# Optimization experiments

Hardware: AMD Instinct MI355X
Metric: run time of the kernel (lower is better)

Reference implementation:

```python
import jax, jax.numpy as jnp
import numpy as np

B, N, C = 8, 1374, 768
H = 12
HD = C // H  # 64
HIDDEN = int(C * 4.0)  # 3072
EPS = 1e-5


def setup_inputs() -> dict:
    key = jax.random.key(0)
    ks = jax.random.split(key, 12)
    s = 0.02
    return {
        "x": jax.random.normal(ks[0], (B, N, C), jnp.float32),
        "rope_freqs": jax.random.normal(ks[1], (1, N, 1, HD), jnp.float32),
        "ln1_g": jnp.ones((C,), jnp.float32),
        "ln1_b": jnp.zeros((C,), jnp.float32),
        "qkv_w": jax.random.normal(ks[2], (3 * C, C), jnp.float32) * s,
        "qkv_b": jnp.zeros((3 * C,), jnp.float32),
        "proj_w": jax.random.normal(ks[3], (C, C), jnp.float32) * s,
        "proj_b": jnp.zeros((C,), jnp.float32),
        "ln2_g": jnp.ones((C,), jnp.float32),
        "ln2_b": jnp.zeros((C,), jnp.float32),
        "w1": jax.random.normal(ks[4], (HIDDEN, C), jnp.float32) * s,
        "b1": jnp.zeros((HIDDEN,), jnp.float32),
        "w2": jax.random.normal(ks[5], (HIDDEN, C), jnp.float32) * s,
        "b2": jnp.zeros((HIDDEN,), jnp.float32),
        "w3": jax.random.normal(ks[6], (C, HIDDEN), jnp.float32) * s,
        "b3": jnp.zeros((C,), jnp.float32),
    }


def _layernorm(x, g, b):
    mu = jnp.mean(x, axis=-1, keepdims=True)
    var = jnp.mean(jnp.square(x - mu), axis=-1, keepdims=True)
    return (x - mu) * jax.lax.rsqrt(var + EPS) * g + b


def _rotate_half(x):
    x1, x2 = jnp.split(x, 2, axis=-1)
    return jnp.concatenate([-x2, x1], axis=-1)


def _apply_rope(q, k, freqs):
    # freqs: [1, N, 1, HD] -> [1, 1, N, HD] (matches torch permute(0,2,1,3))
    f = jnp.transpose(freqs, (0, 2, 1, 3))
    cos, sin = jnp.cos(f), jnp.sin(f)
    q_rot = q * cos + _rotate_half(q) * sin
    k_rot = k * cos + _rotate_half(k) * sin
    return q_rot, k_rot


def reference(x, rope_freqs, ln1_g, ln1_b, qkv_w, qkv_b, proj_w, proj_b,
              ln2_g, ln2_b, w1, b1, w2, b2, w3, b3):
    scale = HD ** -0.5
    # --- Attention branch ---
    h = _layernorm(x, ln1_g, ln1_b)
    qkv = jnp.einsum('bnc,dc->bnd', h, qkv_w) + qkv_b          # [B,N,3C]
    qkv = qkv.reshape(B, N, 3, H, HD).transpose(2, 0, 3, 1, 4)  # [3,B,H,N,HD]
    q, k, v = qkv[0], qkv[1], qkv[2]
    # rope_freqs covers all N tokens -> n_special = 0 path
    q, k = _apply_rope(q, k, rope_freqs)
    attn = jnp.einsum('bhnd,bhmd->bhnm', q, k) * scale          # [B,H,N,N]
    attn = jax.nn.softmax(attn, axis=-1)
    o = jnp.einsum('bhnm,bhmd->bhnd', attn, v)                  # [B,H,N,HD]
    o = o.transpose(0, 2, 1, 3).reshape(B, N, C)
    o = jnp.einsum('bnc,dc->bnd', o, proj_w) + proj_b
    x = x + o
    # --- SwiGLU MLP branch ---
    h2 = _layernorm(x, ln2_g, ln2_b)
    x1 = jnp.einsum('bnc,hc->bnh', h2, w1) + b1
    x2 = jnp.einsum('bnc,hc->bnh', h2, w2) + b2
    hid = jax.nn.silu(x1) * x2
    mlp_out = jnp.einsum('bnh,ch->bnc', hid, w3) + b3
    return x + mlp_out
```

## Files before the change

kernel.cpp:

```cpp
#include <hip/hip_runtime.h>
#include <stdint.h>

#define B_ 8
#define N_ 1374
#define C_ 768
#define H_ 12
#define HD_ 64
#define HID_ 3072
#define M_ (B_*N_)
#define MPAD_ 11008
#define QT_ 22
#define QT2_ 11

#define QSC_ 0.18033688011112042f

typedef __attribute__((ext_vector_type(8))) short short8;
typedef __attribute__((ext_vector_type(4))) float f32x4;
typedef __attribute__((ext_vector_type(16))) float f32x16;
typedef __attribute__((ext_vector_type(4))) _Float16 half4;
typedef __attribute__((ext_vector_type(2))) _Float16 half2v;

__device__ __forceinline__ unsigned short f2bf(float f) {
  unsigned u = __float_as_uint(f);
  u += 0x7FFF + ((u >> 16) & 1);
  return (unsigned short)(u >> 16);
}
__device__ __forceinline__ float bf2f(unsigned short h) {
  return __uint_as_float(((unsigned)h) << 16);
}
__device__ __forceinline__ unsigned short f2h(float f) {
  return __builtin_bit_cast(unsigned short, (_Float16)f);
}

__device__ __forceinline__ half2v pkrtz(float a, float b) {
  return __builtin_bit_cast(half2v, __builtin_amdgcn_cvt_pkrtz(a, b));
}

#if __has_builtin(__builtin_amdgcn_global_load_lds)
#define HAVE_GLL 1
#endif

__device__ __forceinline__ void gld16(const unsigned short* g, unsigned short* l) {
#ifdef HAVE_GLL
  __builtin_amdgcn_global_load_lds((const __attribute__((address_space(1))) void*)g,
                                   (__attribute__((address_space(3))) void*)l, 16, 0, 0);
#else
  *(short8*)l = *(const short8*)g;
#endif
}

__global__ __launch_bounds__(256) void cvt5_kernel(
    const float* __restrict__ s0, const float* __restrict__ s1,
    const float* __restrict__ s2, const float* __restrict__ s3,
    const float* __restrict__ s4, unsigned short* __restrict__ out) {
  int id = blockIdx.x * 256 + threadIdx.x;
  const float* src; int off;
  if (id < 442368)        { src = s0; off = id; }
  else if (id < 589824)   { src = s1; off = id - 442368; }
  else if (id < 1179648)  { src = s2; off = id - 589824; }
  else if (id < 1769472)  { src = s3; off = id - 1179648; }
  else                    { src = s4; off = id - 1769472; }
  float4 v = ((const float4*)src)[off];
  ushort4 o;
  o.x = f2bf(v.x); o.y = f2bf(v.y); o.z = f2bf(v.z); o.w = f2bf(v.w);
  ((ushort4*)out)[id] = o;
}

__global__ __launch_bounds__(256) void ln_kernel(const float* __restrict__ in,
    const float* __restrict__ g, const float* __restrict__ bta,
    unsigned short* __restrict__ out) {
  int row = blockIdx.x;
  int t = threadIdx.x;
  const float* xr = in + (size_t)row * C_;
  float v0 = xr[t], v1 = xr[t + 256], v2 = xr[t + 512];
  float s1 = v0 + v1 + v2;
  float s2 = v0*v0 + v1*v1 + v2*v2;
  for (int off = 1; off < 64; off <<= 1) {
    s1 += __shfl_xor(s1, off, 64);
    s2 += __shfl_xor(s2, off, 64);
  }
  __shared__ float r1[4], r2[4];
  int wave = t >> 6, lane = t & 63;
  if (lane == 0) { r1[wave] = s1; r2[wave] = s2; }
  __syncthreads();
  float tot1 = r1[0] + r1[1] + r1[2] + r1[3];
  float tot2 = r2[0] + r2[1] + r2[2] + r2[3];
  float mu = tot1 * (1.0f / C_);
  float var = tot2 * (1.0f / C_) - mu * mu;
  float rs = rsqrtf(var + 1e-5f);
  size_t ob = (size_t)row * C_;
  out[ob + t]       = f2bf((v0 - mu) * rs * g[t]       + bta[t]);
  out[ob + t + 256] = f2bf((v1 - mu) * rs * g[t + 256] + bta[t + 256]);
  out[ob + t + 512] = f2bf((v2 - mu) * rs * g[t + 512] + bta[t + 512]);
}

template<int EPI, int ROPE, int TM, int SWZ>
__global__ __launch_bounds__(256, (TM == 64) ? 4 : 2) void gemm_bt(
    const unsigned short* __restrict__ A,
    const unsigned short* __restrict__ W,
    void* __restrict__ outp,
    const float* __restrict__ bias0,
    const float* __restrict__ resid,
    const float* __restrict__ freqs,
    int K, int ldo, int Mvalid, int X)
{
  constexpr int MI = TM / 32;
  __shared__ __align__(16) unsigned short As[2][TM * 32];
  __shared__ __align__(16) unsigned short Bs[2][4096];
  const int t = threadIdx.x;
  const int lane = t & 63;
  const int wave = t >> 6;
  const int wm = (wave >> 1) * (TM / 2);
  const int wn = (wave & 1) * 64;
  const int lr = lane & 15;
  const int lg = lane >> 4;
  const int lk = lg * 8;
  int bx, by;
  if (SWZ) {
    int Y = gridDim.x / X;
    int lin = blockIdx.x;
    int sgsz = X * 8;
    int sg = lin / sgsz;
    int base_y = sg * 8;
    int rows = Y - base_y; if (rows > 8) rows = 8;
    int within = lin - sg * sgsz;
    by = base_y + within % rows;
    bx = within / rows;
  } else {
    bx = blockIdx.x % X;
    by = blockIdx.x / X;
  }
  const int tm0 = by * TM;
  const int tn0 = bx * 128;
  const int r0 = t >> 2;
  const int c0 = (t & 3) * 8;
  const unsigned short* ga0 = A + (size_t)(tm0 + r0) * K + c0;
  const unsigned short* ga1 = A + (size_t)(tm0 + 64 + r0) * K + c0;
  const unsigned short* gb0 = W + (size_t)(tn0 + r0) * K + c0;
  const unsigned short* gb1 = W + (size_t)(tn0 + 64 + r0) * K + c0;
  f32x4 zero = {0.f, 0.f, 0.f, 0.f};
  f32x4 acc[MI][4];
#pragma unroll
  for (int mi = 0; mi < MI; ++mi)
#pragma unroll
    for (int ni = 0; ni < 4; ++ni) acc[mi][ni] = zero;

  for (int kt = 0; kt < K; kt += 64) {
    __syncthreads();
    gld16(ga0 + kt,      &As[0][t * 8]);
    gld16(ga0 + kt + 32, &As[1][t * 8]);
    if (TM == 128) {
      gld16(ga1 + kt,      &As[0][2048 + t * 8]);
      gld16(ga1 + kt + 32, &As[1][2048 + t * 8]);
    }
    gld16(gb0 + kt,      &Bs[0][t * 8]);
    gld16(gb1 + kt,      &Bs[0][2048 + t * 8]);
    gld16(gb0 + kt + 32, &Bs[1][t * 8]);
    gld16(gb1 + kt + 32, &Bs[1][2048 + t * 8]);
    __syncthreads();
#pragma unroll
    for (int u = 0; u < 2; ++u) {
      short8 af[MI], bfr[4];
#pragma unroll
      for (int mi = 0; mi < MI; ++mi) af[mi] = *(const short8*)&As[u][(wm + mi * 16 + lr) * 32 + lk];
#pragma unroll
      for (int ni = 0; ni < 4; ++ni) bfr[ni] = *(const short8*)&Bs[u][(wn + ni * 16 + lr) * 32 + lk];
#pragma unroll
      for (int mi = 0; mi < MI; ++mi)
#pragma unroll
        for (int ni = 0; ni < 4; ++ni)
          acc[mi][ni] = __builtin_amdgcn_mfma_f32_16x16x32_bf16(af[mi], bfr[ni], acc[mi][ni], 0, 0, 0);
    }
  }

  if (EPI == 0) {
    bool dorope = ROPE && ((tn0 + wn) < 1536);
    bool isq    = ROPE && ((tn0 + wn) < 768);
    bool isv    = ROPE && ((tn0 + wn) >= 1536);
#pragma unroll
    for (int mi = 0; mi < MI; ++mi) {
#pragma unroll
      for (int p = 0; p < 2; ++p) {
        int col1 = tn0 + wn + p * 16 + lr;
        int col2 = col1 + 32;
        float bv1 = bias0[col1], bv2 = bias0[col2];
        int e = p * 16 + lr;
#pragma unroll
        for (int r = 0; r < 4; ++r) {
          int row = tm0 + wm + mi * 16 + lg * 4 + r;
          float v1 = acc[mi][p][r] + bv1;
          float v2 = acc[mi][p + 2][r] + bv2;
          float o1 = v1, o2 = v2;
          if (dorope) {
            int n = row % N_;
            float f1 = freqs[n * HD_ + e];
            float f2 = freqs[n * HD_ + e + 32];
            float c1, s1, c2, s2;
            __sincosf(f1, &s1, &c1);
            __sincosf(f2, &s2, &c2);
            o1 = v1 * c1 - v2 * s1;
            o2 = v2 * c2 + v1 * s2;
          }
          if (isq) { o1 *= QSC_; o2 *= QSC_; }
          size_t base = (size_t)row * ldo;
          if (isv) {
            ((unsigned short*)outp)[base + col1] = f2h(o1);
            ((unsigned short*)outp)[base + col2] = f2h(o2);
          } else {
            ((unsigned short*)outp)[base + col1] = f2bf(o1);
            ((unsigned short*)outp)[base + col2] = f2bf(o2);
          }
        }
      }
    }
  } else {
#pragma unroll
    for (int mi = 0; mi < MI; ++mi) {
#pragma unroll
      for (int ni = 0; ni < 4; ++ni) {
        int col = tn0 + wn + ni * 16 + lr;
        float bval = bias0[col];
#pragma unroll
        for (int r = 0; r < 4; ++r) {
          int row = tm0 + wm + mi * 16 + lg * 4 + r;
          float v = acc[mi][ni][r] + bval;
          size_t idx = (size_t)row * ldo + col;
          if (EPI == 1) {
            if (row < Mvalid) ((float*)outp)[idx] = resid[idx] + v;
          } else {
            if (row < Mvalid) ((float*)outp)[idx] = ((float*)outp)[idx] + v;
          }
        }
      }
    }
  }
}

__global__ __launch_bounds__(256, 2) void gemm_w12_swiglu(
    const unsigned short* __restrict__ A,
    const unsigned short* __restrict__ W1,
    const unsigned short* __restrict__ W2,
    unsigned short* __restrict__ hid,
    const float* __restrict__ b1,
    const float* __restrict__ b2)
{
  __shared__ __align__(16) unsigned short As[2][4096];
  __shared__ __align__(16) unsigned short B1s[2][2048];
  __shared__ __align__(16) unsigned short B2s[2][2048];
  const int t = threadIdx.x;
  const int lane = t & 63;
  const int wave = t >> 6;
  const int wm = (wave >> 1) * 64;
  const int wn = (wave & 1) * 32;
  const int lr = lane & 15;
  const int lg = lane >> 4;
  const int lk = lg * 8;
  const int tm0 = blockIdx.y * 128;
  const int tn0 = blockIdx.x * 64;
  const int r0 = t >> 2;
  const int c0 = (t & 3) * 8;
  const unsigned short* ga0 = A + (size_t)(tm0 + r0) * 768 + c0;
  const unsigned short* ga1 = A + (size_t)(tm0 + 64 + r0) * 768 + c0;
  const unsigned short* g1 = W1 + (size_t)(tn0 + r0) * 768 + c0;
  const unsigned short* g2 = W2 + (size_t)(tn0 + r0) * 768 + c0;
  f32x4 zero = {0.f, 0.f, 0.f, 0.f};
  f32x4 acc1[4][2], acc2[4][2];
#pragma unroll
  for (int mi = 0; mi < 4; ++mi)
#pragma unroll
    for (int ni = 0; ni < 2; ++ni) { acc1[mi][ni] = zero; acc2[mi][ni] = zero; }

  for (int kt = 0; kt < 768; kt += 64) {
    __syncthreads();
    gld16(ga0 + kt,      &As[0][t * 8]);
    gld16(ga1 + kt,      &As[0][2048 + t * 8]);
    gld16(ga0 + kt + 32, &As[1][t * 8]);
    gld16(ga1 + kt + 32, &As[1][2048 + t * 8]);
    gld16(g1 + kt,       &B1s[0][t * 8]);
    gld16(g1 + kt + 32,  &B1s[1][t * 8]);
    gld16(g2 + kt,       &B2s[0][t * 8]);
    gld16(g2 + kt + 32,  &B2s[1][t * 8]);
    __syncthreads();
#pragma unroll
    for (int u = 0; u < 2; ++u) {
      short8 af[4], b1f[2], b2f[2];
#pragma unroll
      for (int mi = 0; mi < 4; ++mi) af[mi] = *(const short8*)&As[u][(wm + mi * 16 + lr) * 32 + lk];
#pragma unroll
      for (int ni = 0; ni < 2; ++ni) {
        b1f[ni] = *(const short8*)&B1s[u][(wn + ni * 16 + lr) * 32 + lk];
        b2f[ni] = *(const short8*)&B2s[u][(wn + ni * 16 + lr) * 32 + lk];
      }
#pragma unroll
      for (int mi = 0; mi < 4; ++mi)
#pragma unroll
        for (int ni = 0; ni < 2; ++ni) {
          acc1[mi][ni] = __builtin_amdgcn_mfma_f32_16x16x32_bf16(af[mi], b1f[ni], acc1[mi][ni], 0, 0, 0);
          acc2[mi][ni] = __builtin_amdgcn_mfma_f32_16x16x32_bf16(af[mi], b2f[ni], acc2[mi][ni], 0, 0, 0);
        }
    }
  }
#pragma unroll
  for (int mi = 0; mi < 4; ++mi) {
#pragma unroll
    for (int ni = 0; ni < 2; ++ni) {
      int col = tn0 + wn + ni * 16 + lr;
      float bv1 = b1[col], bv2 = b2[col];
#pragma unroll
      for (int r = 0; r < 4; ++r) {
        int row = tm0 + wm + mi * 16 + lg * 4 + r;
        float a1 = acc1[mi][ni][r] + bv1;
        float a2 = acc2[mi][ni][r] + bv2;
        float h = a1 / (1.f + __expf(-a1)) * a2;
        hid[(size_t)row * HID_ + col] = f2bf(h);
      }
    }
  }
}

struct FalseT { static constexpr bool value = false; };
struct TrueT  { static constexpr bool value = true;  };

__global__ __launch_bounds__(256, 3) void attn_kernel(
    const unsigned short* __restrict__ qkv,
    unsigned short* __restrict__ o2)
{
  __shared__ __align__(16) unsigned short Ks[2][64 * 88];
  __shared__ __align__(16) _Float16 Vt[2][64 * 72];
  int bidx = blockIdx.x;
  int qt = bidx % QT2_;
  int bh = bidx / QT2_;
  int head = bh % H_;
  int b = bh / H_;
  int t = threadIdx.x, lane = t & 63, wave = t >> 6;
  int lq = lane & 31, lg2 = lane >> 5;

  short8 bq[4];
  {
    int m = qt * 128 + wave * 32 + lq;
    int mc = (m < N_) ? m : (N_ - 1);
    const unsigned short* qrow = qkv + (size_t)(b * N_ + mc) * 2304 + head * HD_;
#pragma unroll
    for (int c = 0; c < 4; ++c)
      bq[c] = *(const short8*)(qrow + c * 16 + lg2 * 8);
  }

  f32x16 acc[2];
  f32x16 dacc;
  acc[0] = {}; acc[1] = {}; dacc = {};

  const int kr0 = t >> 3;
  const int kc  = (t & 7) * 8;
  const int vp  = t & 31;
  const int vc  = t >> 5;
  const unsigned short* kbase = qkv + (size_t)(b * N_) * 2304 + 768  + head * HD_ + kc;
  const unsigned short* vbase = qkv + (size_t)(b * N_) * 2304 + 1536 + head * HD_ + vc * 8;

  short8 krg[2], vrg[2];
  auto issue = [&](int jt) {
    int j0 = jt * 64 + kr0;        if (j0 >= N_) j0 = N_ - 1;
    int j1 = jt * 64 + kr0 + 32;   if (j1 >= N_) j1 = N_ - 1;
    int vj0 = jt * 64 + 2 * vp;    if (vj0 >= N_) vj0 = N_ - 1;
    int vj1 = jt * 64 + 2 * vp + 1; if (vj1 >= N_) vj1 = N_ - 1;
    krg[0] = *(const short8*)(kbase + (size_t)j0 * 2304);
    krg[1] = *(const short8*)(kbase + (size_t)j1 * 2304);
    vrg[0] = *(const short8*)(vbase + (size_t)vj0 * 2304);
    vrg[1] = *(const short8*)(vbase + (size_t)vj1 * 2304);
  };

  const half4 vones = {(_Float16)1.f, (_Float16)1.f, (_Float16)1.f, (_Float16)1.f};

  auto compute = [&](int jt, const unsigned short* ksb, const _Float16* vtb, auto tailc) {
    constexpr bool TAIL = decltype(tailc)::value;
#pragma unroll
    for (int st2 = 0; st2 < 2; ++st2) {
      f32x16 sc = {};
      {
        const unsigned short* krow = &ksb[(st2 * 32 + lq) * 88 + lg2 * 8];
        short8 ak0 = *(const short8*)(krow);
        short8 ak1 = *(const short8*)(krow + 16);
        short8 ak2 = *(const short8*)(krow + 32);
        short8 ak3 = *(const short8*)(krow + 48);
        sc = __builtin_amdgcn_mfma_f32_32x32x16_bf16(ak0, bq[0], sc, 0, 0, 0);
        sc = __builtin_amdgcn_mfma_f32_32x32x16_bf16(ak1, bq[1], sc, 0, 0, 0);
        sc = __builtin_amdgcn_mfma_f32_32x32x16_bf16(ak2, bq[2], sc, 0, 0, 0);
        sc = __builtin_amdgcn_mfma_f32_32x32x16_bf16(ak3, bq[3], sc, 0, 0, 0);
      }
#pragma unroll
      for (int r = 0; r < 16; ++r) {
        float pv = exp2f(sc[r]);
        if (TAIL) {
          int jw = (r & 3) + 8 * (r >> 2) + 4 * lg2;
          int j = jt * 64 + st2 * 32 + jw;
          pv = (j < N_) ? pv : 0.f;
        }
        sc[r] = pv;
      }
      half4 pf[4];
#pragma unroll
      for (int ks = 0; ks < 4; ++ks) {
        union { half4 v; half2v h[2]; } pu;
        pu.h[0] = pkrtz(sc[ks * 4 + 0], sc[ks * 4 + 1]);
        pu.h[1] = pkrtz(sc[ks * 4 + 2], sc[ks * 4 + 3]);
        pf[ks] = pu.v;
      }
#pragma unroll
      for (int ks = 0; ks < 4; ++ks)
        dacc = __builtin_amdgcn_mfma_f32_32x32x8f16(pf[ks], vones, dacc, 0, 0, 0);
#pragma unroll
      for (int dt = 0; dt < 2; ++dt) {
#pragma unroll
        for (int ks = 0; ks < 4; ++ks) {
          half4 bv = *(const half4*)&vtb[(dt * 32 + lq) * 72 + st2 * 32 + ks * 8 + lg2 * 4];
          acc[dt] = __builtin_amdgcn_mfma_f32_32x32x8f16(pf[ks], bv, acc[dt], 0, 0, 0);
        }
      }
    }
  };

  issue(0);
  int cur = 0;
  for (int jt = 0; jt < QT_; ++jt) {
    unsigned short* ksb = &Ks[cur][0];
    _Float16* vtb = &Vt[cur][0];
    *(short8*)&ksb[kr0 * 88 + kc] = krg[0];
    *(short8*)&ksb[(kr0 + 32) * 88 + kc] = krg[1];
#pragma unroll
    for (int i = 0; i < 8; ++i) {
      unsigned lo = (unsigned short)vrg[0][i];
      unsigned hi = (unsigned short)vrg[1][i];
      *(unsigned*)&Vt[cur][(vc * 8 + i) * 72 + 2 * vp] = lo | (hi << 16);
    }
    __syncthreads();
    issue(jt + 1);
    if (jt == QT_ - 1) compute(jt, ksb, vtb, TrueT{});
    else               compute(jt, ksb, vtb, FalseT{});
    cur ^= 1;
  }

#pragma unroll
  for (int r = 0; r < 16; ++r) {
    int qw = (r & 3) + 8 * (r >> 2) + 4 * lg2;
    int m = qt * 128 + wave * 32 + qw;
    if (m < N_) {
      float invd = 1.f / dacc[r];
      unsigned short* orow = o2 + (size_t)(b * N_ + m) * C_ + head * HD_ + lq;
      orow[0]  = f2bf(acc[0][r] * invd);
      orow[32] = f2bf(acc[1][r] * invd);
    }
  }
}

extern "C" void kernel_launch(void* const* d_in, const int* in_sizes, int n_in,
                              void* d_out, int out_size, void* d_ws, size_t ws_size,
                              hipStream_t stream) {
  const float* x      = (const float*)d_in[0];
  const float* freqs  = (const float*)d_in[1];
  const float* ln1_g  = (const float*)d_in[2];
  const float* ln1_b  = (const float*)d_in[3];
  const float* qkv_w  = (const float*)d_in[4];
  const float* qkv_b  = (const float*)d_in[5];
  const float* proj_w = (const float*)d_in[6];
  const float* proj_b = (const float*)d_in[7];
  const float* ln2_g  = (const float*)d_in[8];
  const float* ln2_b  = (const float*)d_in[9];
  const float* w1     = (const float*)d_in[10];
  const float* b1     = (const float*)d_in[11];
  const float* w2     = (const float*)d_in[12];
  const float* b2     = (const float*)d_in[13];
  const float* w3     = (const float*)d_in[14];
  const float* b3     = (const float*)d_in[15];
  float* out = (float*)d_out;
  char* ws = (char*)d_ws;

  unsigned short* hB     = (unsigned short*)(ws + 0);
  unsigned short* wqkvB  = (unsigned short*)(ws + 16908288);
  unsigned short* wprojB = (unsigned short*)(ws + 20447232);
  unsigned short* w12B   = (unsigned short*)(ws + 21626880);
  unsigned short* w3B    = (unsigned short*)(ws + 31064064);
  unsigned short* qkvB   = (unsigned short*)(ws + 35782656);
  unsigned short* o2B    = (unsigned short*)(ws + 86507520);
  unsigned short* hidB   = qkvB;

  cvt5_kernel<<<9216, 256, 0, stream>>>(qkv_w, proj_w, w1, w2, w3, wqkvB);

  ln_kernel<<<M_, 256, 0, stream>>>(x, ln1_g, ln1_b, hB);
  gemm_bt<0, 1, 128, 1><<<18 * 86, 256, 0, stream>>>(hB, wqkvB, qkvB, qkv_b, nullptr, freqs, 768, 2304, M_, 18);
  attn_kernel<<<B_ * H_ * QT2_, 256, 0, stream>>>(qkvB, o2B);
  gemm_bt<1, 0, 64, 1><<<6 * 172, 256, 0, stream>>>(o2B, wprojB, out, proj_b, x, nullptr, 768, 768, M_, 6);

  ln_kernel<<<M_, 256, 0, stream>>>(out, ln2_g, ln2_b, hB);
  gemm_w12_swiglu<<<dim3(48, 86), 256, 0, stream>>>(hB, w12B, w12B + 3072 * 768, hidB, b1, b2);
  gemm_bt<3, 0, 128, 1><<<6 * 86, 256, 0, stream>>>(hidB, w3B, out, b3, nullptr, nullptr, 3072, 768, M_, 6);
}
```

Baseline: 534.5 us.

## Double-buffer LDS tiles in GEMM kernels to overlap global loads with MFMA

Both the generic GEMM and the fused W1/W2 SwiGLU GEMM now keep two LDS stages. The next K-tile is issued into the alternate buffer while MFMAs run on the current one, which also drops one barrier per iteration. The goal is to hide global-to-LDS load latency behind compute. The cost is double the LDS footprint per block, so the TM=64 launch bound drops from 4 to 3 blocks per CU, which can reduce occupancy.

```diff
diff --git a/kernel.cpp b/kernel.cpp
--- a/kernel.cpp
+++ b/kernel.cpp
@@ -95,7 +95,7 @@
 }
 
 template<int EPI, int ROPE, int TM, int SWZ>
-__global__ __launch_bounds__(256, (TM == 64) ? 4 : 2) void gemm_bt(
+__global__ __launch_bounds__(256, (TM == 64) ? 3 : 2) void gemm_bt(
     const unsigned short* __restrict__ A,
     const unsigned short* __restrict__ W,
     void* __restrict__ outp,
@@ -105,8 +105,8 @@
     int K, int ldo, int Mvalid, int X)
 {
   constexpr int MI = TM / 32;
-  __shared__ __align__(16) unsigned short As[2][TM * 32];
-  __shared__ __align__(16) unsigned short Bs[2][4096];
+  __shared__ __align__(16) unsigned short As[2][2][TM * 32];
+  __shared__ __align__(16) unsigned short Bs[2][2][4096];
   const int t = threadIdx.x;
   const int lane = t & 63;
   const int wave = t >> 6;
@@ -138,6 +138,20 @@
   const unsigned short* ga1 = A + (size_t)(tm0 + 64 + r0) * K + c0;
   const unsigned short* gb0 = W + (size_t)(tn0 + r0) * K + c0;
   const unsigned short* gb1 = W + (size_t)(tn0 + 64 + r0) * K + c0;
+
+  auto stage = [&](int buf, int kt) {
+    gld16(ga0 + kt,      &As[buf][0][t * 8]);
+    gld16(ga0 + kt + 32, &As[buf][1][t * 8]);
+    if (TM == 128) {
+      gld16(ga1 + kt,      &As[buf][0][2048 + t * 8]);
+      gld16(ga1 + kt + 32, &As[buf][1][2048 + t * 8]);
+    }
+    gld16(gb0 + kt,      &Bs[buf][0][t * 8]);
+    gld16(gb1 + kt,      &Bs[buf][0][2048 + t * 8]);
+    gld16(gb0 + kt + 32, &Bs[buf][1][t * 8]);
+    gld16(gb1 + kt + 32, &Bs[buf][1][2048 + t * 8]);
+  };
+
   f32x4 zero = {0.f, 0.f, 0.f, 0.f};
   f32x4 acc[MI][4];
 #pragma unroll
@@ -145,32 +159,25 @@
 #pragma unroll
     for (int ni = 0; ni < 4; ++ni) acc[mi][ni] = zero;
 
+  stage(0, 0);
+  int cur = 0;
   for (int kt = 0; kt < K; kt += 64) {
     __syncthreads();
-    gld16(ga0 + kt,      &As[0][t * 8]);
-    gld16(ga0 + kt + 32, &As[1][t * 8]);
-    if (TM == 128) {
-      gld16(ga1 + kt,      &As[0][2048 + t * 8]);
-      gld16(ga1 + kt + 32, &As[1][2048 + t * 8]);
-    }
-    gld16(gb0 + kt,      &Bs[0][t * 8]);
-    gld16(gb1 + kt,      &Bs[0][2048 + t * 8]);
-    gld16(gb0 + kt + 32, &Bs[1][t * 8]);
-    gld16(gb1 + kt + 32, &Bs[1][2048 + t * 8]);
-    __syncthreads();
+    if (kt + 64 < K) stage(cur ^ 1, kt + 64);
 #pragma unroll
     for (int u = 0; u < 2; ++u) {
       short8 af[MI], bfr[4];
 #pragma unroll
-      for (int mi = 0; mi < MI; ++mi) af[mi] = *(const short8*)&As[u][(wm + mi * 16 + lr) * 32 + lk];
-#pragma unroll
-      for (int ni = 0; ni < 4; ++ni) bfr[ni] = *(const short8*)&Bs[u][(wn + ni * 16 + lr) * 32 + lk];
+      for (int mi = 0; mi < MI; ++mi) af[mi] = *(const short8*)&As[cur][u][(wm + mi * 16 + lr) * 32 + lk];
+#pragma unroll
+      for (int ni = 0; ni < 4; ++ni) bfr[ni] = *(const short8*)&Bs[cur][u][(wn + ni * 16 + lr) * 32 + lk];
 #pragma unroll
       for (int mi = 0; mi < MI; ++mi)
 #pragma unroll
         for (int ni = 0; ni < 4; ++ni)
           acc[mi][ni] = __builtin_amdgcn_mfma_f32_16x16x32_bf16(af[mi], bfr[ni], acc[mi][ni], 0, 0, 0);
     }
+    cur ^= 1;
   }
 
   if (EPI == 0) {
@@ -244,9 +251,9 @@
     const float* __restrict__ b1,
     const float* __restrict__ b2)
 {
-  __shared__ __align__(16) unsigned short As[2][4096];
-  __shared__ __align__(16) unsigned short B1s[2][2048];
-  __shared__ __align__(16) unsigned short B2s[2][2048];
+  __shared__ __align__(16) unsigned short As[2][2][4096];
+  __shared__ __align__(16) unsigned short B1s[2][2][2048];
+  __shared__ __align__(16) unsigned short B2s[2][2][2048];
   const int t = threadIdx.x;
   const int lane = t & 63;
   const int wave = t >> 6;
@@ -263,6 +270,18 @@
   const unsigned short* ga1 = A + (size_t)(tm0 + 64 + r0) * 768 + c0;
   const unsigned short* g1 = W1 + (size_t)(tn0 + r0) * 768 + c0;
   const unsigned short* g2 = W2 + (size_t)(tn0 + r0) * 768 + c0;
+
+  auto stage = [&](int buf, int kt) {
+    gld16(ga0 + kt,      &As[buf][0][t * 8]);
+    gld16(ga1 + kt,      &As[buf][0][2048 + t * 8]);
+    gld16(ga0 + kt + 32, &As[buf][1][t * 8]);
+    gld16(ga1 + kt + 32, &As[buf][1][2048 + t * 8]);
+    gld16(g1 + kt,       &B1s[buf][0][t * 8]);
+    gld16(g1 + kt + 32,  &B1s[buf][1][t * 8]);
+    gld16(g2 + kt,       &B2s[buf][0][t * 8]);
+    gld16(g2 + kt + 32,  &B2s[buf][1][t * 8]);
+  };
+
   f32x4 zero = {0.f, 0.f, 0.f, 0.f};
   f32x4 acc1[4][2], acc2[4][2];
 #pragma unroll
@@ -270,26 +289,20 @@
 #pragma unroll
     for (int ni = 0; ni < 2; ++ni) { acc1[mi][ni] = zero; acc2[mi][ni] = zero; }
 
+  stage(0, 0);
+  int cur = 0;
   for (int kt = 0; kt < 768; kt += 64) {
     __syncthreads();
-    gld16(ga0 + kt,      &As[0][t * 8]);
-    gld16(ga1 + kt,      &As[0][2048 + t * 8]);
-    gld16(ga0 + kt + 32, &As[1][t * 8]);
-    gld16(ga1 + kt + 32, &As[1][2048 + t * 8]);
-    gld16(g1 + kt,       &B1s[0][t * 8]);
-    gld16(g1 + kt + 32,  &B1s[1][t * 8]);
-    gld16(g2 + kt,       &B2s[0][t * 8]);
-    gld16(g2 + kt + 32,  &B2s[1][t * 8]);
-    __syncthreads();
+    if (kt + 64 < 768) stage(cur ^ 1, kt + 64);
 #pragma unroll
     for (int u = 0; u < 2; ++u) {
       short8 af[4], b1f[2], b2f[2];
 #pragma unroll
-      for (int mi = 0; mi < 4; ++mi) af[mi] = *(const short8*)&As[u][(wm + mi * 16 + lr) * 32 + lk];
+      for (int mi = 0; mi < 4; ++mi) af[mi] = *(const short8*)&As[cur][u][(wm + mi * 16 + lr) * 32 + lk];
 #pragma unroll
       for (int ni = 0; ni < 2; ++ni) {
-        b1f[ni] = *(const short8*)&B1s[u][(wn + ni * 16 + lr) * 32 + lk];
-        b2f[ni] = *(const short8*)&B2s[u][(wn + ni * 16 + lr) * 32 + lk];
+        b1f[ni] = *(const short8*)&B1s[cur][u][(wn + ni * 16 + lr) * 32 + lk];
+        b2f[ni] = *(const short8*)&B2s[cur][u][(wn + ni * 16 + lr) * 32 + lk];
       }
 #pragma unroll
       for (int mi = 0; mi < 4; ++mi)
@@ -299,6 +312,7 @@
           acc2[mi][ni] = __builtin_amdgcn_mfma_f32_16x16x32_bf16(af[mi], b2f[ni], acc2[mi][ni], 0, 0, 0);
         }
     }
+    cur ^= 1;
   }
 #pragma unroll
   for (int mi = 0; mi < 4; ++mi) {
```

Result: slower. 643.1 us (+20.3%).

## Double-buffer LDS tiles in the GEMM and SwiGLU kernels to overlap loads with MFMA

Applied to the files above, without the earlier changes.

The main GEMM and the fused SwiGLU up-projection kernel now use a software-pipelined K loop. The two LDS buffers hold consecutive 32-wide K slices instead of two halves of one 64-wide slice. Each iteration issues the global-to-LDS loads for the next slice and then runs MFMAs on the current one, with a single barrier per step. The goal is to hide global load latency behind matrix math. The cost is twice as many loop iterations and barriers, and each step has less MFMA work to cover the load latency.

```diff
diff --git a/kernel.cpp b/kernel.cpp
--- a/kernel.cpp
+++ b/kernel.cpp
@@ -138,6 +138,14 @@
   const unsigned short* ga1 = A + (size_t)(tm0 + 64 + r0) * K + c0;
   const unsigned short* gb0 = W + (size_t)(tn0 + r0) * K + c0;
   const unsigned short* gb1 = W + (size_t)(tn0 + 64 + r0) * K + c0;
+
+  auto stage = [&](int buf, int kt) {
+    gld16(ga0 + kt, &As[buf][t * 8]);
+    if (TM == 128) gld16(ga1 + kt, &As[buf][2048 + t * 8]);
+    gld16(gb0 + kt, &Bs[buf][t * 8]);
+    gld16(gb1 + kt, &Bs[buf][2048 + t * 8]);
+  };
+
   f32x4 zero = {0.f, 0.f, 0.f, 0.f};
   f32x4 acc[MI][4];
 #pragma unroll
@@ -145,32 +153,22 @@
 #pragma unroll
     for (int ni = 0; ni < 4; ++ni) acc[mi][ni] = zero;
 
-  for (int kt = 0; kt < K; kt += 64) {
+  stage(0, 0);
+  int cur = 0;
+  for (int kt = 0; kt < K; kt += 32) {
     __syncthreads();
-    gld16(ga0 + kt,      &As[0][t * 8]);
-    gld16(ga0 + kt + 32, &As[1][t * 8]);
-    if (TM == 128) {
-      gld16(ga1 + kt,      &As[0][2048 + t * 8]);
-      gld16(ga1 + kt + 32, &As[1][2048 + t * 8]);
-    }
-    gld16(gb0 + kt,      &Bs[0][t * 8]);
-    gld16(gb1 + kt,      &Bs[0][2048 + t * 8]);
-    gld16(gb0 + kt + 32, &Bs[1][t * 8]);
-    gld16(gb1 + kt + 32, &Bs[1][2048 + t * 8]);
-    __syncthreads();
-#pragma unroll
-    for (int u = 0; u < 2; ++u) {
-      short8 af[MI], bfr[4];
-#pragma unroll
-      for (int mi = 0; mi < MI; ++mi) af[mi] = *(const short8*)&As[u][(wm + mi * 16 + lr) * 32 + lk];
-#pragma unroll
-      for (int ni = 0; ni < 4; ++ni) bfr[ni] = *(const short8*)&Bs[u][(wn + ni * 16 + lr) * 32 + lk];
-#pragma unroll
-      for (int mi = 0; mi < MI; ++mi)
-#pragma unroll
-        for (int ni = 0; ni < 4; ++ni)
-          acc[mi][ni] = __builtin_amdgcn_mfma_f32_16x16x32_bf16(af[mi], bfr[ni], acc[mi][ni], 0, 0, 0);
-    }
+    if (kt + 32 < K) stage(cur ^ 1, kt + 32);
+    short8 af[MI], bfr[4];
+#pragma unroll
+    for (int mi = 0; mi < MI; ++mi) af[mi] = *(const short8*)&As[cur][(wm + mi * 16 + lr) * 32 + lk];
+#pragma unroll
+    for (int ni = 0; ni < 4; ++ni) bfr[ni] = *(const short8*)&Bs[cur][(wn + ni * 16 + lr) * 32 + lk];
+#pragma unroll
+    for (int mi = 0; mi < MI; ++mi)
+#pragma unroll
+      for (int ni = 0; ni < 4; ++ni)
+        acc[mi][ni] = __builtin_amdgcn_mfma_f32_16x16x32_bf16(af[mi], bfr[ni], acc[mi][ni], 0, 0, 0);
+    cur ^= 1;
   }
 
   if (EPI == 0) {
@@ -263,6 +261,14 @@
   const unsigned short* ga1 = A + (size_t)(tm0 + 64 + r0) * 768 + c0;
   const unsigned short* g1 = W1 + (size_t)(tn0 + r0) * 768 + c0;
   const unsigned short* g2 = W2 + (size_t)(tn0 + r0) * 768 + c0;
+
+  auto stage = [&](int buf, int kt) {
+    gld16(ga0 + kt, &As[buf][t * 8]);
+    gld16(ga1 + kt, &As[buf][2048 + t * 8]);
+    gld16(g1 + kt,  &B1s[buf][t * 8]);
+    gld16(g2 + kt,  &B2s[buf][t * 8]);
+  };
+
   f32x4 zero = {0.f, 0.f, 0.f, 0.f};
   f32x4 acc1[4][2], acc2[4][2];
 #pragma unroll
@@ -270,35 +276,27 @@
 #pragma unroll
     for (int ni = 0; ni < 2; ++ni) { acc1[mi][ni] = zero; acc2[mi][ni] = zero; }
 
-  for (int kt = 0; kt < 768; kt += 64) {
+  stage(0, 0);
+  int cur = 0;
+  for (int kt = 0; kt < 768; kt += 32) {
     __syncthreads();
-    gld16(ga0 + kt,      &As[0][t * 8]);
-    gld16(ga1 + kt,      &As[0][2048 + t * 8]);
-    gld16(ga0 + kt + 32, &As[1][t * 8]);
-    gld16(ga1 + kt + 32, &As[1][2048 + t * 8]);
-    gld16(g1 + kt,       &B1s[0][t * 8]);
-    gld16(g1 + kt + 32,  &B1s[1][t * 8]);
-    gld16(g2 + kt,       &B2s[0][t * 8]);
-    gld16(g2 + kt + 32,  &B2s[1][t * 8]);
-    __syncthreads();
-#pragma unroll
-    for (int u = 0; u < 2; ++u) {
-      short8 af[4], b1f[2], b2f[2];
-#pragma unroll
-      for (int mi = 0; mi < 4; ++mi) af[mi] = *(const short8*)&As[u][(wm + mi * 16 + lr) * 32 + lk];
+    if (kt + 32 < 768) stage(cur ^ 1, kt + 32);
+    short8 af[4], b1f[2], b2f[2];
+#pragma unroll
+    for (int mi = 0; mi < 4; ++mi) af[mi] = *(const short8*)&As[cur][(wm + mi * 16 + lr) * 32 + lk];
+#pragma unroll
+    for (int ni = 0; ni < 2; ++ni) {
+      b1f[ni] = *(const short8*)&B1s[cur][(wn + ni * 16 + lr) * 32 + lk];
+      b2f[ni] = *(const short8*)&B2s[cur][(wn + ni * 16 + lr) * 32 + lk];
+    }
+#pragma unroll
+    for (int mi = 0; mi < 4; ++mi)
 #pragma unroll
       for (int ni = 0; ni < 2; ++ni) {
-        b1f[ni] = *(const short8*)&B1s[u][(wn + ni * 16 + lr) * 32 + lk];
-        b2f[ni] = *(const short8*)&B2s[u][(wn + ni * 16 + lr) * 32 + lk];
-      }
-#pragma unroll
-      for (int mi = 0; mi < 4; ++mi)
-#pragma unroll
-        for (int ni = 0; ni < 2; ++ni) {
-          acc1[mi][ni] = __builtin_amdgcn_mfma_f32_16x16x32_bf16(af[mi], b1f[ni], acc1[mi][ni], 0, 0, 0);
-          acc2[mi][ni] = __builtin_amdgcn_mfma_f32_16x16x32_bf16(af[mi], b2f[ni], acc2[mi][ni], 0, 0, 0);
-        }
-    }
+        acc1[mi][ni] = __builtin_amdgcn_mfma_f32_16x16x32_bf16(af[mi], b1f[ni], acc1[mi][ni], 0, 0, 0);
+        acc2[mi][ni] = __builtin_amdgcn_mfma_f32_16x16x32_bf16(af[mi], b2f[ni], acc2[mi][ni], 0, 0, 0);
+      }
+    cur ^= 1;
   }
 #pragma unroll
   for (int mi = 0; mi < 4; ++mi) {
```

New measurement: 598.9 us. 12.0% more time.
